# Optimization experiments

Hardware: AMD Instinct MI355X
Metric: run time of the kernel (lower is better)

## Reference

```python
import jax, jax.numpy as jnp
import numpy as np

# PointPillars KITTI grid
NX, NY, NZ = 432, 496, 1
C = 64            # num_bev_features
B = 8             # batch size
P_PER = 4096      # pillars per sample (<=4096 -> deterministic path, no gumbel gating)
GRID = NZ * NX * NY


def setup_inputs() -> dict:
    key = jax.random.key(0)
    pillar_features = jax.random.normal(key, (B * P_PER, C), dtype=jnp.float32)
    # Unique flat indices per sample: stride 53 is coprime with NX*NY=214272,
    # and P_PER < NX*NY, so all indices within a sample are distinct (scatter-set safe).
    flat = (np.arange(P_PER, dtype=np.int64) * 53) % (NX * NY)
    ys = flat // NX
    xs = flat % NX
    coords = np.stack([
        np.repeat(np.arange(B, dtype=np.int64), P_PER),  # batch index
        np.zeros(B * P_PER, dtype=np.int64),             # z (always 0, nz==1)
        np.tile(ys, B),                                  # y
        np.tile(xs, B),                                  # x
    ], axis=1)
    return {
        "pillar_features": pillar_features,
        "voxel_coords": jnp.asarray(coords, dtype=jnp.int32),
    }


def reference(pillar_features, voxel_coords):
    c = voxel_coords.astype(jnp.int32)
    # per-sample flat index into the nz*nx*ny canvas: z + y*nx + x
    idx = c[:, 1] + c[:, 2] * NX + c[:, 3]
    # fold batch into a single global scatter (one kernel instead of a per-batch loop)
    gidx = c[:, 0] * GRID + idx                       # [P]
    canvas = jnp.zeros((B * GRID, C), dtype=pillar_features.dtype)
    canvas = canvas.at[gidx].set(pillar_features)     # sparse-to-dense scatter
    # [B*GRID, C] -> [B, GRID, C] -> [B, C, GRID] -> [B, C*nz, ny, nx]
    out = canvas.reshape(B, GRID, C).transpose(0, 2, 1).reshape(B, C * NZ, NY, NX)
    return out
```

## Files before the change

### kernel.cpp

```cpp
#include <hip/hip_runtime.h>


#define PPS_NX   432
#define PPS_NY   496
#define PPS_GRID (PPS_NX * PPS_NY)
#define PPS_C    64
#define PPS_B    8
#define PPS_U    (PPS_GRID / 4)

__global__ void pps_init_map(int4* __restrict__ map4, int n4) {
    int i = blockIdx.x * blockDim.x + threadIdx.x;
    if (i < n4) map4[i] = make_int4(-1, -1, -1, -1);
}

__global__ void pps_scatter_idx(const int4* __restrict__ coords,
                                int* __restrict__ map, int P) {
    int p = blockIdx.x * blockDim.x + threadIdx.x;
    if (p >= P) return;
    int4 c = coords[p];
    int pos = c.y + c.z * PPS_NX + c.w;
    map[c.x * PPS_GRID + pos] = p;
}

__global__ void pps_gather(const float* __restrict__ pf,
                           const int* __restrict__ map,
                           float* __restrict__ out) {
    int t = blockIdx.x * blockDim.x + threadIdx.x;
    int b = t / PPS_U;
    int u = t - b * PPS_U;

    int4 m = ((const int4*)(map + b * PPS_GRID))[u];
    float* ob = out + (long long)b * (PPS_C * (long long)PPS_GRID) + 4 * u;

    const float4 z4 = make_float4(0.f, 0.f, 0.f, 0.f);
    for (int ch0 = 0; ch0 < PPS_C; ch0 += 4) {
        float4 p0 = z4, p1 = z4, p2 = z4, p3 = z4;
        if (m.x >= 0) p0 = *(const float4*)(pf + (long long)m.x * PPS_C + ch0);
        if (m.y >= 0) p1 = *(const float4*)(pf + (long long)m.y * PPS_C + ch0);
        if (m.z >= 0) p2 = *(const float4*)(pf + (long long)m.z * PPS_C + ch0);
        if (m.w >= 0) p3 = *(const float4*)(pf + (long long)m.w * PPS_C + ch0);

        float* o0 = ob + (long long)(ch0 + 0) * PPS_GRID;
        float* o1 = ob + (long long)(ch0 + 1) * PPS_GRID;
        float* o2 = ob + (long long)(ch0 + 2) * PPS_GRID;
        float* o3 = ob + (long long)(ch0 + 3) * PPS_GRID;
        *(float4*)o0 = make_float4(p0.x, p1.x, p2.x, p3.x);
        *(float4*)o1 = make_float4(p0.y, p1.y, p2.y, p3.y);
        *(float4*)o2 = make_float4(p0.z, p1.z, p2.z, p3.z);
        *(float4*)o3 = make_float4(p0.w, p1.w, p2.w, p3.w);
    }
}

__global__ void pps_zero_out(float4* __restrict__ out, long long n4) {
    long long i = (long long)blockIdx.x * blockDim.x + threadIdx.x;
    const long long stride = (long long)gridDim.x * blockDim.x;
    const float4 z = make_float4(0.f, 0.f, 0.f, 0.f);
    for (; i < n4; i += stride) out[i] = z;
}
__global__ void pps_scatter_feat(const float* __restrict__ pf,
                                 const int4* __restrict__ coords,
                                 float* __restrict__ out, int P) {
    int t = blockIdx.x * blockDim.x + threadIdx.x;
    int p = t >> 6;
    if (p >= P) return;
    int ch = t & 63;
    int4 c = coords[p];
    long long pos = (long long)c.x * (long long)(PPS_C * PPS_GRID)
                  + (long long)ch * PPS_GRID
                  + (long long)(c.y + c.z * PPS_NX + c.w);
    out[pos] = pf[t];
}

extern "C" void kernel_launch(void* const* d_in, const int* in_sizes, int n_in,
                              void* d_out, int out_size, void* d_ws, size_t ws_size,
                              hipStream_t stream) {
    const float* pf     = (const float*)d_in[0];
    const int4*  coords = (const int4*)d_in[1];
    float*       out    = (float*)d_out;
    int P = in_sizes[0] / PPS_C;

    const size_t map_bytes = (size_t)PPS_B * PPS_GRID * sizeof(int);
    if (ws_size >= map_bytes) {
        int* map = (int*)d_ws;
        int n4 = PPS_B * PPS_U;
        pps_init_map<<<(n4 + 255) / 256, 256, 0, stream>>>((int4*)map, n4);
        pps_scatter_idx<<<(P + 255) / 256, 256, 0, stream>>>(coords, map, P);
        pps_gather<<<PPS_B * PPS_U / 256, 256, 0, stream>>>(pf, map, out);
    } else {
        long long n4 = (long long)out_size / 4;
        pps_zero_out<<<2048, 256, 0, stream>>>((float4*)out, n4);
        int threads = P * PPS_C;
        pps_scatter_feat<<<(threads + 255) / 256, 256, 0, stream>>>(pf, coords, out, P);
    }
}
```

Measured before the change: 438.8 us.

## Restructure gather to one thread per output float4 across channel planes

Replaces the gather kernel, where each thread looped over all 64 channels for four grid cells, with a flat kernel in which each thread writes exactly one float4 of the output in linear order. Each thread works out its batch, channel and cell group, reads the int4 pillar map entry, and loads feature scalars only when some cell in the group is occupied. This aims to raise memory-level parallelism and give perfectly sequential streaming writes over the huge, mostly-zero output. The cost is that every map entry is re-read once per channel (64 times, ideally served from cache), and feature loads become scalar rather than float4.

```diff
diff --git a/kernel.cpp b/kernel.cpp
--- a/kernel.cpp
+++ b/kernel.cpp
@@ -7,6 +7,8 @@
 #define PPS_C    64
 #define PPS_B    8
 #define PPS_U    (PPS_GRID / 4)
+
+typedef float f32x4 __attribute__((ext_vector_type(4)));
 
 __global__ void pps_init_map(int4* __restrict__ map4, int n4) {
     int i = blockIdx.x * blockDim.x + threadIdx.x;
@@ -22,33 +24,25 @@
     map[c.x * PPS_GRID + pos] = p;
 }
 
-__global__ void pps_gather(const float* __restrict__ pf,
-                           const int* __restrict__ map,
-                           float* __restrict__ out) {
-    int t = blockIdx.x * blockDim.x + threadIdx.x;
-    int b = t / PPS_U;
-    int u = t - b * PPS_U;
+__global__ __launch_bounds__(256) void pps_write(const float* __restrict__ pf,
+                                                 const int* __restrict__ map,
+                                                 f32x4* __restrict__ out4) {
+    int f = blockIdx.x * 256 + threadIdx.x;
+    int plane = (unsigned)f / PPS_U;
+    int u = f - plane * PPS_U;
+    int b = plane >> 6;
+    int ch = plane & 63;
 
-    int4 m = ((const int4*)(map + b * PPS_GRID))[u];
-    float* ob = out + (long long)b * (PPS_C * (long long)PPS_GRID) + 4 * u;
+    const int4 m = ((const int4*)(map + (size_t)b * PPS_GRID))[u];
 
-    const float4 z4 = make_float4(0.f, 0.f, 0.f, 0.f);
-    for (int ch0 = 0; ch0 < PPS_C; ch0 += 4) {
-        float4 p0 = z4, p1 = z4, p2 = z4, p3 = z4;
-        if (m.x >= 0) p0 = *(const float4*)(pf + (long long)m.x * PPS_C + ch0);
-        if (m.y >= 0) p1 = *(const float4*)(pf + (long long)m.y * PPS_C + ch0);
-        if (m.z >= 0) p2 = *(const float4*)(pf + (long long)m.z * PPS_C + ch0);
-        if (m.w >= 0) p3 = *(const float4*)(pf + (long long)m.w * PPS_C + ch0);
-
-        float* o0 = ob + (long long)(ch0 + 0) * PPS_GRID;
-        float* o1 = ob + (long long)(ch0 + 1) * PPS_GRID;
-        float* o2 = ob + (long long)(ch0 + 2) * PPS_GRID;
-        float* o3 = ob + (long long)(ch0 + 3) * PPS_GRID;
-        *(float4*)o0 = make_float4(p0.x, p1.x, p2.x, p3.x);
-        *(float4*)o1 = make_float4(p0.y, p1.y, p2.y, p3.y);
-        *(float4*)o2 = make_float4(p0.z, p1.z, p2.z, p3.z);
-        *(float4*)o3 = make_float4(p0.w, p1.w, p2.w, p3.w);
+    f32x4 v = {0.f, 0.f, 0.f, 0.f};
+    if ((m.x & m.y & m.z & m.w) >= 0) {
+        if (m.x >= 0) v.x = pf[(size_t)m.x * PPS_C + ch];
+        if (m.y >= 0) v.y = pf[(size_t)m.y * PPS_C + ch];
+        if (m.z >= 0) v.z = pf[(size_t)m.z * PPS_C + ch];
+        if (m.w >= 0) v.w = pf[(size_t)m.w * PPS_C + ch];
     }
+    out4[f] = v;
 }
 
 __global__ void pps_zero_out(float4* __restrict__ out, long long n4) {
@@ -85,7 +79,8 @@
         int n4 = PPS_B * PPS_U;
         pps_init_map<<<(n4 + 255) / 256, 256, 0, stream>>>((int4*)map, n4);
         pps_scatter_idx<<<(P + 255) / 256, 256, 0, stream>>>(coords, map, P);
-        pps_gather<<<PPS_B * PPS_U / 256, 256, 0, stream>>>(pf, map, out);
+        int total4 = out_size / 4;
+        pps_write<<<total4 / 256, 256, 0, stream>>>(pf, map, (f32x4*)out);
     } else {
         long long n4 = (long long)out_size / 4;
         pps_zero_out<<<2048, 256, 0, stream>>>((float4*)out, n4);
```

Result: no change. 435.9 us (-0.6%).
